# Performance work log

Measured on AMD Instinct MI355X. Metric: run time of the kernel, lower is better.

## Reference

```python
import jax, jax.numpy as jnp
import numpy as np

B, L, D, H, NL, EXP = 8, 1024, 512, 8, 6, 4
DH = D // H
DF = D * EXP
EPS = 1e-3  # keras LayerNormalization default epsilon
NEG = -1e9  # keras Softmax mask adder for float32


def _ln(x, g, b):
    m = jnp.mean(x, axis=-1, keepdims=True)
    v = jnp.mean(jnp.square(x - m), axis=-1, keepdims=True)
    return (x - m) * jax.lax.rsqrt(v + EPS) * g + b


def _pos_emb(L, D):
    pos = jnp.arange(L, dtype=jnp.float32)[:, None]          # [L,1]
    i = jnp.arange(D // 2, dtype=jnp.float32)[None, :]        # [1,D/2]
    inv = jnp.power(10000.0, -2.0 * i / D)
    # original concatenates sin block then cos block along feature axis
    return jnp.concatenate([jnp.sin(pos * inv), jnp.cos(pos * inv)], axis=-1)  # [L,D]


def setup_inputs() -> dict:
    key = jax.random.key(0)
    ks = jax.random.split(key, 16)
    glorot = lambda k, shape: jax.random.uniform(
        k, shape, jnp.float32, -1.0, 1.0) * jnp.sqrt(6.0 / (shape[-2] + shape[-1]))
    return {
        "x": jax.random.normal(ks[0], (B, L, D), jnp.float32),
        "lengths": jax.random.randint(ks[1], (B,), L // 2, L + 1).astype(jnp.int32),
        "Wq": glorot(ks[2], (NL, D, D)),
        "Wk": glorot(ks[3], (NL, D, D)),
        "Wv": glorot(ks[4], (NL, D, D)),
        "Wo": glorot(ks[5], (NL, D, D)),
        "ln1_g": jnp.ones((NL, D), jnp.float32),
        "ln1_b": jnp.zeros((NL, D), jnp.float32),
        "ln2_g": jnp.ones((NL, D), jnp.float32),
        "ln2_b": jnp.zeros((NL, D), jnp.float32),
        "w1": glorot(ks[6], (NL, D, DF)),
        "b1": jnp.zeros((NL, DF), jnp.float32),
        "w2": glorot(ks[7], (NL, DF, D)),
        "b2": jnp.zeros((NL, D), jnp.float32),
    }


def _forward(x, mask_bias, Wq, Wk, Wv, Wo, ln1_g, ln1_b, ln2_g, ln2_b, w1, b1, w2, b2):
    x = x + _pos_emb(L, D)[None, :, :]
    scale = 1.0 / jnp.sqrt(jnp.float32(DH))

    def layer(x, p):
        wq, wk, wv, wo, g1, be1, g2, be2, fw1, fb1, fw2, fb2 = p
        h = _ln(x, g1, be1)
        split = lambda t: t.reshape(B, L, H, DH).transpose(0, 2, 1, 3)  # [B,H,L,DH]
        q, k, v = split(h @ wq), split(h @ wk), split(h @ wv)
        scores = jnp.einsum("bhqd,bhkd->bhqk", q, k) * scale + mask_bias
        attn = jax.nn.softmax(scores, axis=-1)
        o = jnp.einsum("bhqk,bhkd->bhqd", attn, v)
        o = o.transpose(0, 2, 1, 3).reshape(B, L, D) @ wo
        x = x + o  # dropout is identity at inference
        h2 = _ln(x, g2, be2)
        ffn = jax.nn.relu(h2 @ fw1 + fb1) @ fw2 + fb2
        return x + ffn, None

    x, _ = jax.lax.scan(layer, x, (Wq, Wk, Wv, Wo, ln1_g, ln1_b, ln2_g, ln2_b, w1, b1, w2, b2))
    return x


def reference(x, lengths, Wq, Wk, Wv, Wo, ln1_g, ln1_b, ln2_g, ln2_b, w1, b1, w2, b2):
    mask = (jnp.arange(L)[None, :] < lengths[:, None]).astype(jnp.float32)  # [B,L]
    mask_bias = (1.0 - mask)[:, None, None, :] * NEG                        # [B,1,1,L]
    return _forward(x, mask_bias, Wq, Wk, Wv, Wo, ln1_g, ln1_b, ln2_g, ln2_b, w1, b1, w2, b2)
```

## Files before the change

kernel.cpp:

```cpp
#include <hip/hip_runtime.h>
#include <cstdint>
#include <cstddef>

#define Bz 8
#define Lz 1024
#define Dz 512
#define Hz 8
#define NLz 6
#define DFz 2048
#define Mz (Bz*Lz)

typedef short bf16x8 __attribute__((ext_vector_type(8)));
typedef float f32x4  __attribute__((ext_vector_type(4)));

__device__ __forceinline__ short f2bf(float f) {
    unsigned u = __builtin_bit_cast(unsigned, f);
    u = (u + 0x7fff + ((u >> 16) & 1)) >> 16;
    return (short)u;
}

__device__ __forceinline__ float exp2_fast(float x) {
#if __has_builtin(__builtin_amdgcn_exp2f)
    return __builtin_amdgcn_exp2f(x);
#else
    return exp2f(x);
#endif
}

#define GLD16(gp, lp) __builtin_amdgcn_global_load_lds( \
    (const __attribute__((address_space(1))) void*)(gp), \
    (__attribute__((address_space(3))) void*)(lp), 16, 0, 0)

__global__ __launch_bounds__(256) void posadd_kernel(const float* __restrict__ x,
                                                     float* __restrict__ y) {
    int idx = blockIdx.x * 256 + threadIdx.x;
    int d   = idx & (Dz - 1);
    int pos = (idx >> 9) & (Lz - 1);
    int i2  = (d < Dz/2) ? d : d - Dz/2;
    float inv = __expf(-0.03597789207f * (float)i2);
    float a = (float)pos * inv;
    float pe = (d < Dz/2) ? sinf(a) : cosf(a);
    y[idx] = x[idx] + pe;
}

__global__ __launch_bounds__(256) void ln_kernel(const float* __restrict__ x,
                                                 const float* __restrict__ g,
                                                 const float* __restrict__ b,
                                                 short* __restrict__ out) {
    int row = blockIdx.x;
    int t = threadIdx.x;
    const float* xr = x + (size_t)row * Dz;
    float v0 = xr[t], v1 = xr[t + 256];
    float s = v0 + v1;
    #pragma unroll
    for (int off = 32; off; off >>= 1) s += __shfl_xor(s, off, 64);
    __shared__ float red[4];
    int w = t >> 6, l = t & 63;
    if (l == 0) red[w] = s;
    __syncthreads();
    float m = (red[0] + red[1] + red[2] + red[3]) * (1.0f / Dz);
    float d0 = v0 - m, d1 = v1 - m;
    float s2 = d0 * d0 + d1 * d1;
    #pragma unroll
    for (int off = 32; off; off >>= 1) s2 += __shfl_xor(s2, off, 64);
    __syncthreads();
    if (l == 0) red[w] = s2;
    __syncthreads();
    float var = (red[0] + red[1] + red[2] + red[3]) * (1.0f / Dz);
    float rs = rsqrtf(var + 1e-3f);
    out[(size_t)row * Dz + t]       = f2bf(d0 * rs * g[t] + b[t]);
    out[(size_t)row * Dz + t + 256] = f2bf(d1 * rs * g[t + 256] + b[t + 256]);
}

__global__ __launch_bounds__(256) void transpose_bf16_kernel(const float* __restrict__ src,
                                                             short* __restrict__ dst,
                                                             int K, int N,
                                                             long srcLS, long dstLS, int rowOff) {
    __shared__ float tile[32][33];
    int tx = threadIdx.x & 31, ty = threadIdx.x >> 5;
    int bx = blockIdx.x, by = blockIdx.y, z = blockIdx.z;
    const float* s = src + (size_t)z * srcLS;
    short* d = dst + (size_t)z * dstLS;
    #pragma unroll
    for (int i = 0; i < 4; i++)
        tile[ty + i * 8][tx] = s[(size_t)(by * 32 + ty + i * 8) * N + bx * 32 + tx];
    __syncthreads();
    #pragma unroll
    for (int i = 0; i < 4; i++)
        d[(size_t)(rowOff + bx * 32 + ty + i * 8) * K + by * 32 + tx] = f2bf(tile[tx][ty + i * 8]);
}

__global__ __launch_bounds__(256) void vtrans_kernel(const short* __restrict__ qkv,
                                                     short* __restrict__ vbt) {
    int lt = blockIdx.x, bh = blockIdx.y;
    int b = bh >> 3, h = bh & 7;
    __shared__ short tile[64][72];
    int t = threadIdx.x;
    int l = t >> 2, c4 = t & 3;
    #pragma unroll
    for (int p = 0; p < 2; p++) {
        int dd = (c4 + p * 4) * 8;
        *(uint4*)&tile[l][dd] =
            *(const uint4*)(qkv + ((size_t)(b * Lz + lt * 64 + l)) * 1536 + 1024 + h * 64 + dd);
    }
    __syncthreads();
    int d = t >> 2;
    #pragma unroll
    for (int p = 0; p < 2; p++) {
        int lc = (c4 + p * 4) * 8;
        union { uint4 u; short s[8]; } o;
        #pragma unroll
        for (int j = 0; j < 8; j++) o.s[j] = tile[lc + j][d];
        *(uint4*)(vbt + ((size_t)(bh * 64 + d)) * Lz + lt * 64 + lc) = o.u;
    }
}

template<int MODE, int TN>
__global__ __launch_bounds__(256, 2)
void gemm_bt(const short* __restrict__ A,
             const short* __restrict__ Bt,
             short* __restrict__ outb,
             float* __restrict__ outf,
             const float* __restrict__ bias,
             int M, int N, int K) {
    constexpr int NI = TN / 32;
    __shared__ __attribute__((aligned(16))) short As[128 * 64];
    __shared__ __attribute__((aligned(16))) short Bs[TN * 64];
    int t = threadIdx.x;
    int m0 = blockIdx.x * 128, n0 = blockIdx.y * TN;
    int w = t >> 6, l = t & 63;
    int wm = (w >> 1) * 64, wn = (w & 1) * (TN / 2);
    int lr = l & 15, lq = l >> 4;
    f32x4 acc[4][NI] = {};
    int sr = t >> 3;
    int sc = ((t & 7) ^ (sr & 7)) * 8;
    for (int kk = 0; kk < K; kk += 64) {
        #pragma unroll
        for (int i = 0; i < 4; i++)
            GLD16(A + (size_t)(m0 + sr + i * 32) * K + kk + sc, As + i * 2048 + t * 8);
        #pragma unroll
        for (int i = 0; i < TN / 32; i++)
            GLD16(Bt + (size_t)(n0 + sr + i * 32) * K + kk + sc, Bs + i * 2048 + t * 8);
        __syncthreads();
        bf16x8 af[4][2], bfr[NI][2];
        #pragma unroll
        for (int i = 0; i < 4; i++) {
            int row = wm + i * 16 + lr;
            const short* rp = As + row * 64;
            af[i][0] = *(const bf16x8*)(rp + ((lq ^ (row & 7)) * 8));
            af[i][1] = *(const bf16x8*)(rp + (((4 + lq) ^ (row & 7)) * 8));
        }
        #pragma unroll
        for (int i = 0; i < NI; i++) {
            int row = wn + i * 16 + lr;
            const short* rp = Bs + row * 64;
            bfr[i][0] = *(const bf16x8*)(rp + ((lq ^ (row & 7)) * 8));
            bfr[i][1] = *(const bf16x8*)(rp + (((4 + lq) ^ (row & 7)) * 8));
        }
        #pragma unroll
        for (int mi = 0; mi < 4; mi++)
            #pragma unroll
            for (int ni = 0; ni < NI; ni++) {
                acc[mi][ni] = __builtin_amdgcn_mfma_f32_16x16x32_bf16(af[mi][0], bfr[ni][0], acc[mi][ni], 0, 0, 0);
                acc[mi][ni] = __builtin_amdgcn_mfma_f32_16x16x32_bf16(af[mi][1], bfr[ni][1], acc[mi][ni], 0, 0, 0);
            }
        __syncthreads();
    }
    #pragma unroll
    for (int mi = 0; mi < 4; mi++)
        #pragma unroll
        for (int ni = 0; ni < NI; ni++) {
            int col = n0 + wn + ni * 16 + lr;
            float bv = (MODE == 2 || MODE == 3) ? bias[col] : 0.0f;
            #pragma unroll
            for (int r = 0; r < 4; r++) {
                int row = m0 + wm + mi * 16 + lq * 4 + r;
                size_t idx = (size_t)row * N + col;
                float v = acc[mi][ni][r];
                if (MODE == 0)      outb[idx] = f2bf(v);
                else if (MODE == 1) outf[idx] += v;
                else if (MODE == 2) outb[idx] = f2bf(fmaxf(v + bv, 0.0f));
                else                outf[idx] += v + bv;
            }
        }
}

__device__ __forceinline__ void attn_frag(f32x4* sacc, const float* biask,
                                          float* mr, float* lsum, f32x4* oacc,
                                          short* Pw, const short* Vs,
                                          int lr, int lq, bf16x8 onesf) {
    const float SC2 = 0.18033688f;
    float p[8][4];
    #pragma unroll
    for (int r = 0; r < 4; r++) {
        float mx = -1e30f;
        #pragma unroll
        for (int kt = 0; kt < 8; kt++) {
            p[kt][r] = sacc[kt][r] * SC2 + biask[kt];
            mx = fmaxf(mx, p[kt][r]);
        }
        mx = fmaxf(mx, __shfl_xor(mx, 1, 64));
        mx = fmaxf(mx, __shfl_xor(mx, 2, 64));
        mx = fmaxf(mx, __shfl_xor(mx, 4, 64));
        mx = fmaxf(mx, __shfl_xor(mx, 8, 64));
        float mn = fmaxf(mr[r], mx);
        float alpha = exp2_fast(mr[r] - mn);
        mr[r] = mn;
        #pragma unroll
        for (int kt = 0; kt < 8; kt++)
            p[kt][r] = exp2_fast(p[kt][r] - mn);
        lsum[r] *= alpha;
        #pragma unroll
        for (int ni = 0; ni < 4; ni++) oacc[ni][r] *= alpha;
    }
    #pragma unroll
    for (int kt = 0; kt < 8; kt++)
        #pragma unroll
        for (int r = 0; r < 4; r++)
            Pw[(lq * 4 + r) * 136 + kt * 16 + lr] = f2bf(p[kt][r]);
    f32x4 sums = {};
    #pragma unroll
    for (int c = 0; c < 4; c++) {
        bf16x8 pf = *(const bf16x8*)(Pw + lr * 136 + c * 32 + lq * 8);
        sums = __builtin_amdgcn_mfma_f32_16x16x32_bf16(pf, onesf, sums, 0, 0, 0);
        #pragma unroll
        for (int ni = 0; ni < 4; ni++) {
            bf16x8 vf = *(const bf16x8*)(Vs + (ni * 16 + lr) * 136 + c * 32 + lq * 8);
            oacc[ni] = __builtin_amdgcn_mfma_f32_16x16x32_bf16(pf, vf, oacc[ni], 0, 0, 0);
        }
    }
    #pragma unroll
    for (int r = 0; r < 4; r++) lsum[r] += sums[r];
}

__global__ __launch_bounds__(256, 2) void attn_kernel(const short* __restrict__ qkv,
                                                      const short* __restrict__ vbt,
                                                      const int* __restrict__ lengths,
                                                      short* __restrict__ o) {
    __shared__ __attribute__((aligned(16))) short Ks[128 * 72];
    __shared__ __attribute__((aligned(16))) short Vs[64 * 136];
    __shared__ __attribute__((aligned(16))) short Ps[4][16 * 136];
    int qt = blockIdx.y;
    int bh = blockIdx.x;
    int b = bh >> 3, h = bh & 7;
    int len = lengths[b];
    int t = threadIdx.x, w = t >> 6, l = t & 63;
    int lr = l & 15, lq = l >> 4;

    const short* q0 = qkv + (size_t)(b * Lz + qt * 128 + w * 32 + lr) * 1536 + h * 64 + lq * 8;
    bf16x8 qf0a = *(const bf16x8*)(q0);
    bf16x8 qf0b = *(const bf16x8*)(q0 + 32);
    bf16x8 qf1a = *(const bf16x8*)(q0 + 16 * 1536);
    bf16x8 qf1b = *(const bf16x8*)(q0 + 16 * 1536 + 32);

    int kkey = t >> 3, kd8 = (t & 7) * 8;
    int vd = t >> 4, vk8 = (t & 15) * 8;
    const short* kbaseg = qkv + (size_t)(b * Lz) * 1536 + 512 + h * 64;
    const short* vbaseg = vbt + (size_t)(bh * 64) * Lz;

    float mr0[4] = {-1e30f, -1e30f, -1e30f, -1e30f}, ls0[4] = {0.f, 0.f, 0.f, 0.f};
    float mr1[4] = {-1e30f, -1e30f, -1e30f, -1e30f}, ls1[4] = {0.f, 0.f, 0.f, 0.f};
    f32x4 oacc0[4] = {}, oacc1[4] = {};
    bf16x8 onesf = {0x3F80, 0x3F80, 0x3F80, 0x3F80, 0x3F80, 0x3F80, 0x3F80, 0x3F80};

    uint4 kreg[4], vreg[4];
    #pragma unroll
    for (int i = 0; i < 4; i++)
        kreg[i] = *(const uint4*)(kbaseg + (size_t)(i * 32 + kkey) * 1536 + kd8);

    short* Pw = &Ps[w][0];
    int ntiles = (len + 127) >> 7;
    for (int tix = 0; tix < ntiles; tix++) {
        int k0 = tix << 7;
        __syncthreads();
        #pragma unroll
        for (int i = 0; i < 4; i++)
            *(uint4*)(Ks + (i * 32 + kkey) * 72 + kd8) = kreg[i];
        __syncthreads();
        #pragma unroll
        for (int i = 0; i < 4; i++)
            vreg[i] = *(const uint4*)(vbaseg + (size_t)(i * 16 + vd) * Lz + k0 + vk8);
        f32x4 sacc[8] = {};
        #pragma unroll
        for (int kt = 0; kt < 8; kt++) {
            bf16x8 kf0 = *(const bf16x8*)(Ks + (kt * 16 + lr) * 72 + lq * 8);
            bf16x8 kf1 = *(const bf16x8*)(Ks + (kt * 16 + lr) * 72 + 32 + lq * 8);
            sacc[kt] = __builtin_amdgcn_mfma_f32_16x16x32_bf16(qf0a, kf0, sacc[kt], 0, 0, 0);
            sacc[kt] = __builtin_amdgcn_mfma_f32_16x16x32_bf16(qf0b, kf1, sacc[kt], 0, 0, 0);
        }
        if (tix + 1 < ntiles) {
            #pragma unroll
            for (int i = 0; i < 4; i++)
                kreg[i] = *(const uint4*)(kbaseg + (size_t)(k0 + 128 + i * 32 + kkey) * 1536 + kd8);
        }
        #pragma unroll
        for (int i = 0; i < 4; i++)
            *(uint4*)(Vs + (i * 16 + vd) * 136 + vk8) = vreg[i];
        float biask[8];
        #pragma unroll
        for (int kt = 0; kt < 8; kt++)
            biask[kt] = ((k0 + kt * 16 + lr) < len) ? 0.0f : -1e30f;
        __syncthreads();
        attn_frag(sacc, biask, mr0, ls0, oacc0, Pw, Vs, lr, lq, onesf);
        #pragma unroll
        for (int kt = 0; kt < 8; kt++) {
            bf16x8 kf0 = *(const bf16x8*)(Ks + (kt * 16 + lr) * 72 + lq * 8);
            bf16x8 kf1 = *(const bf16x8*)(Ks + (kt * 16 + lr) * 72 + 32 + lq * 8);
            f32x4 s2 = {};
            s2 = __builtin_amdgcn_mfma_f32_16x16x32_bf16(qf1a, kf0, s2, 0, 0, 0);
            s2 = __builtin_amdgcn_mfma_f32_16x16x32_bf16(qf1b, kf1, s2, 0, 0, 0);
            sacc[kt] = s2;
        }
        attn_frag(sacc, biask, mr1, ls1, oacc1, Pw, Vs, lr, lq, onesf);
    }
    #pragma unroll
    for (int ni = 0; ni < 4; ni++)
        #pragma unroll
        for (int r = 0; r < 4; r++) {
            int q = qt * 128 + w * 32 + lq * 4 + r;
            size_t base = (size_t)(b * Lz + q) * Dz + h * 64 + ni * 16 + lr;
            o[base]             = f2bf(oacc0[ni][r] / ls0[r]);
            o[base + 16 * Dz]   = f2bf(oacc1[ni][r] / ls1[r]);
        }
}

extern "C" void kernel_launch(void* const* d_in, const int* in_sizes, int n_in,
                              void* d_out, int out_size, void* d_ws, size_t ws_size,
                              hipStream_t stream) {
    const float* x_in    = (const float*)d_in[0];
    const int*   lengths = (const int*)d_in[1];
    const float* Wq   = (const float*)d_in[2];
    const float* Wk   = (const float*)d_in[3];
    const float* Wv   = (const float*)d_in[4];
    const float* Wo   = (const float*)d_in[5];
    const float* ln1g = (const float*)d_in[6];
    const float* ln1b = (const float*)d_in[7];
    const float* ln2g = (const float*)d_in[8];
    const float* ln2b = (const float*)d_in[9];
    const float* w1   = (const float*)d_in[10];
    const float* b1   = (const float*)d_in[11];
    const float* w2   = (const float*)d_in[12];
    const float* b2   = (const float*)d_in[13];

    size_t off = 0;
    auto alloc = [&](size_t bytes) {
        void* p = (char*)d_ws + off;
        off += (bytes + 255) & ~(size_t)255;
        return p;
    };
    float* x_work = (float*)alloc((size_t)Mz * Dz * 4);
    short* hbuf   = (short*)alloc((size_t)Mz * Dz * 2);
    short* qkvb   = (short*)alloc((size_t)Mz * 1536 * 2);
    short* f1b    = (short*)alloc((size_t)Mz * DFz * 2);
    short* vbt    = (short*)alloc((size_t)Bz * Hz * 64 * Lz * 2);
    short* wqkvT  = (short*)alloc((size_t)NLz * 1536 * Dz * 2);
    short* woT    = (short*)alloc((size_t)NLz * Dz * Dz * 2);
    short* w1T    = (short*)alloc((size_t)NLz * DFz * Dz * 2);
    short* w2T    = (short*)alloc((size_t)NLz * Dz * DFz * 2);

    dim3 tb(256);
    transpose_bf16_kernel<<<dim3(16, 16, NLz), tb, 0, stream>>>(Wq, wqkvT, Dz, Dz, (long)Dz*Dz, (long)1536*Dz, 0);
    transpose_bf16_kernel<<<dim3(16, 16, NLz), tb, 0, stream>>>(Wk, wqkvT, Dz, Dz, (long)Dz*Dz, (long)1536*Dz, 512);
    transpose_bf16_kernel<<<dim3(16, 16, NLz), tb, 0, stream>>>(Wv, wqkvT, Dz, Dz, (long)Dz*Dz, (long)1536*Dz, 1024);
    transpose_bf16_kernel<<<dim3(16, 16, NLz), tb, 0, stream>>>(Wo, woT, Dz, Dz, (long)Dz*Dz, (long)Dz*Dz, 0);
    transpose_bf16_kernel<<<dim3(64, 16, NLz), tb, 0, stream>>>(w1, w1T, Dz, DFz, (long)Dz*DFz, (long)DFz*Dz, 0);
    transpose_bf16_kernel<<<dim3(16, 64, NLz), tb, 0, stream>>>(w2, w2T, DFz, Dz, (long)DFz*Dz, (long)Dz*DFz, 0);

    posadd_kernel<<<dim3(Mz * Dz / 256), tb, 0, stream>>>(x_in, x_work);

    for (int lyr = 0; lyr < NLz; lyr++) {
        const short* wqkvL = wqkvT + (size_t)lyr * 1536 * Dz;
        const short* woL   = woT   + (size_t)lyr * Dz * Dz;
        const short* w1L   = w1T   + (size_t)lyr * DFz * Dz;
        const short* w2L   = w2T   + (size_t)lyr * Dz * DFz;

        ln_kernel<<<dim3(Mz), tb, 0, stream>>>(x_work, ln1g + lyr * Dz, ln1b + lyr * Dz, hbuf);
        gemm_bt<0,128><<<dim3(Mz/128, 1536/128), tb, 0, stream>>>(hbuf, wqkvL, qkvb, nullptr, nullptr, Mz, 1536, Dz);
        vtrans_kernel<<<dim3(Lz/64, Bz*Hz), tb, 0, stream>>>(qkvb, vbt);
        attn_kernel<<<dim3(Bz*Hz, Lz/128), tb, 0, stream>>>(qkvb, vbt, lengths, hbuf);
        gemm_bt<1,64><<<dim3(Mz/128, Dz/64), tb, 0, stream>>>(hbuf, woL, nullptr, x_work, nullptr, Mz, Dz, Dz);
        ln_kernel<<<dim3(Mz), tb, 0, stream>>>(x_work, ln2g + lyr * Dz, ln2b + lyr * Dz, hbuf);
        gemm_bt<2,128><<<dim3(Mz/128, DFz/128), tb, 0, stream>>>(hbuf, w1L, f1b, nullptr, b1 + lyr * DFz, Mz, DFz, Dz);
        gemm_bt<3,64><<<dim3(Mz/128, Dz/64), tb, 0, stream>>>(f1b, w2L, nullptr, x_work, b2 + lyr * Dz, Mz, Dz, DFz);
    }

    hipMemcpyAsync(d_out, x_work, (size_t)Mz * Dz * 4, hipMemcpyDeviceToDevice, stream);
}
```

Baseline: 1.087 ms.

## Double-buffer GEMM LDS tiles and fuse final residual write into output

```diff
diff --git a/kernel.cpp b/kernel.cpp
--- a/kernel.cpp
+++ b/kernel.cpp
@@ -116,16 +116,19 @@
 }
 
 template<int MODE, int TN>
-__global__ __launch_bounds__(256, 2)
+__global__ __launch_bounds__(256, (TN == 64) ? 3 : 2)
 void gemm_bt(const short* __restrict__ A,
              const short* __restrict__ Bt,
              short* __restrict__ outb,
              float* __restrict__ outf,
+             float* __restrict__ outf2,
              const float* __restrict__ bias,
              int M, int N, int K) {
     constexpr int NI = TN / 32;
-    __shared__ __attribute__((aligned(16))) short As[128 * 64];
-    __shared__ __attribute__((aligned(16))) short Bs[TN * 64];
+    constexpr int ASZ = 128 * 64;
+    constexpr int BSZ = TN * 64;
+    __shared__ __attribute__((aligned(16))) short As[2 * ASZ];
+    __shared__ __attribute__((aligned(16))) short Bs[2 * BSZ];
     int t = threadIdx.x;
     int m0 = blockIdx.x * 128, n0 = blockIdx.y * TN;
     int w = t >> 6, l = t & 63;
@@ -134,26 +137,32 @@
     f32x4 acc[4][NI] = {};
     int sr = t >> 3;
     int sc = ((t & 7) ^ (sr & 7)) * 8;
-    for (int kk = 0; kk < K; kk += 64) {
+
+    auto stage = [&](int cur, int kk) {
+        short* Ad = As + cur * ASZ;
+        short* Bd = Bs + cur * BSZ;
         #pragma unroll
         for (int i = 0; i < 4; i++)
-            GLD16(A + (size_t)(m0 + sr + i * 32) * K + kk + sc, As + i * 2048 + t * 8);
+            GLD16(A + (size_t)(m0 + sr + i * 32) * K + kk + sc, Ad + i * 2048 + t * 8);
         #pragma unroll
         for (int i = 0; i < TN / 32; i++)
-            GLD16(Bt + (size_t)(n0 + sr + i * 32) * K + kk + sc, Bs + i * 2048 + t * 8);
-        __syncthreads();
+            GLD16(Bt + (size_t)(n0 + sr + i * 32) * K + kk + sc, Bd + i * 2048 + t * 8);
+    };
+    auto compute = [&](int cur) {
+        const short* Ab = As + cur * ASZ;
+        const short* Bb = Bs + cur * BSZ;
         bf16x8 af[4][2], bfr[NI][2];
         #pragma unroll
         for (int i = 0; i < 4; i++) {
             int row = wm + i * 16 + lr;
-            const short* rp = As + row * 64;
+            const short* rp = Ab + row * 64;
             af[i][0] = *(const bf16x8*)(rp + ((lq ^ (row & 7)) * 8));
             af[i][1] = *(const bf16x8*)(rp + (((4 + lq) ^ (row & 7)) * 8));
         }
         #pragma unroll
         for (int i = 0; i < NI; i++) {
             int row = wn + i * 16 + lr;
-            const short* rp = Bs + row * 64;
+            const short* rp = Bb + row * 64;
             bfr[i][0] = *(const bf16x8*)(rp + ((lq ^ (row & 7)) * 8));
             bfr[i][1] = *(const bf16x8*)(rp + (((4 + lq) ^ (row & 7)) * 8));
         }
@@ -164,14 +173,26 @@
                 acc[mi][ni] = __builtin_amdgcn_mfma_f32_16x16x32_bf16(af[mi][0], bfr[ni][0], acc[mi][ni], 0, 0, 0);
                 acc[mi][ni] = __builtin_amdgcn_mfma_f32_16x16x32_bf16(af[mi][1], bfr[ni][1], acc[mi][ni], 0, 0, 0);
             }
+    };
+
+    int nt = K >> 6;
+    stage(0, 0);
+    __syncthreads();
+    int cur = 0;
+    for (int tix = 0; tix < nt - 1; ++tix) {
+        stage(cur ^ 1, (tix + 1) << 6);
+        compute(cur);
         __syncthreads();
-    }
+        cur ^= 1;
+    }
+    compute(cur);
+
     #pragma unroll
     for (int mi = 0; mi < 4; mi++)
         #pragma unroll
         for (int ni = 0; ni < NI; ni++) {
             int col = n0 + wn + ni * 16 + lr;
-            float bv = (MODE == 2 || MODE == 3) ? bias[col] : 0.0f;
+            float bv = (MODE == 2 || MODE == 3 || MODE == 4) ? bias[col] : 0.0f;
             #pragma unroll
             for (int r = 0; r < 4; r++) {
                 int row = m0 + wm + mi * 16 + lq * 4 + r;
@@ -180,7 +201,8 @@
                 if (MODE == 0)      outb[idx] = f2bf(v);
                 else if (MODE == 1) outf[idx] += v;
                 else if (MODE == 2) outb[idx] = f2bf(fmaxf(v + bv, 0.0f));
-                else                outf[idx] += v + bv;
+                else if (MODE == 3) outf[idx] += v + bv;
+                else                outf2[idx] = outf[idx] + v + bv;
             }
         }
 }
@@ -375,14 +397,15 @@
         const short* w2L   = w2T   + (size_t)lyr * Dz * DFz;
 
         ln_kernel<<<dim3(Mz), tb, 0, stream>>>(x_work, ln1g + lyr * Dz, ln1b + lyr * Dz, hbuf);
-        gemm_bt<0,128><<<dim3(Mz/128, 1536/128), tb, 0, stream>>>(hbuf, wqkvL, qkvb, nullptr, nullptr, Mz, 1536, Dz);
+        gemm_bt<0,128><<<dim3(Mz/128, 1536/128), tb, 0, stream>>>(hbuf, wqkvL, qkvb, nullptr, nullptr, nullptr, Mz, 1536, Dz);
         vtrans_kernel<<<dim3(Lz/64, Bz*Hz), tb, 0, stream>>>(qkvb, vbt);
         attn_kernel<<<dim3(Bz*Hz, Lz/128), tb, 0, stream>>>(qkvb, vbt, lengths, hbuf);
-        gemm_bt<1,64><<<dim3(Mz/128, Dz/64), tb, 0, stream>>>(hbuf, woL, nullptr, x_work, nullptr, Mz, Dz, Dz);
+        gemm_bt<1,64><<<dim3(Mz/128, Dz/64), tb, 0, stream>>>(hbuf, woL, nullptr, x_work, nullptr, nullptr, Mz, Dz, Dz);
         ln_kernel<<<dim3(Mz), tb, 0, stream>>>(x_work, ln2g + lyr * Dz, ln2b + lyr * Dz, hbuf);
-        gemm_bt<2,128><<<dim3(Mz/128, DFz/128), tb, 0, stream>>>(hbuf, w1L, f1b, nullptr, b1 + lyr * DFz, Mz, DFz, Dz);
-        gemm_bt<3,64><<<dim3(Mz/128, Dz/64), tb, 0, stream>>>(f1b, w2L, nullptr, x_work, b2 + lyr * Dz, Mz, Dz, DFz);
-    }
-
-    hipMemcpyAsync(d_out, x_work, (size_t)Mz * Dz * 4, hipMemcpyDeviceToDevice, stream);
-}
+        gemm_bt<2,128><<<dim3(Mz/128, DFz/128), tb, 0, stream>>>(hbuf, w1L, f1b, nullptr, nullptr, b1 + lyr * DFz, Mz, DFz, Dz);
+        if (lyr < NLz - 1)
+            gemm_bt<3,64><<<dim3(Mz/128, Dz/64), tb, 0, stream>>>(f1b, w2L, nullptr, x_work, nullptr, b2 + lyr * Dz, Mz, Dz, DFz);
+        else
+            gemm_bt<4,64><<<dim3(Mz/128, Dz/64), tb, 0, stream>>>(f1b, w2L, nullptr, x_work, (float*)d_out, b2 + lyr * Dz, Mz, Dz, DFz);
+    }
+}
```

Result: slower. 1.240 ms (+14.0%).
